# Optimization experiments

Hardware: AMD Instinct MI355X
Metric: run time of the kernel (lower is better)

Reference implementation:

```python
import jax, jax.numpy as jnp
import numpy as np

IGNORE_INDEX = -100


def setup_inputs() -> dict:
    key = jax.random.key(0)
    k1, k2, k3 = jax.random.split(key, 3)
    BT, H, V = 4096, 2048, 32000
    hidden_states = jax.random.normal(k1, (BT, H), dtype=jnp.float32) * 0.02
    weight = jax.random.normal(k2, (V, H), dtype=jnp.float32) * 0.02
    targets = jax.random.randint(k3, (BT,), 0, V, dtype=jnp.int64)
    return {"hidden_states": hidden_states, "weight": weight, "targets": targets}


def reference(hidden_states, weight, targets):
    # Fused lm_head projection + cross-entropy with ignore_index masking,
    # 'mean' reduction over valid rows (matches reduction='mean').
    logits = jnp.einsum('bh,vh->bv', hidden_states, weight).astype(jnp.float32)  # (BT, V)
    lse = jax.nn.logsumexp(logits, axis=-1)  # (BT,)
    safe_tgt = jnp.clip(targets, 0, logits.shape[-1] - 1)
    target_logit = jnp.take_along_axis(logits, safe_tgt[:, None], axis=-1)[:, 0]
    valid = targets != IGNORE_INDEX
    loss_rows = jnp.where(valid, lse - target_logit, 0.0)  # (BT,)
    n_valid = jnp.maximum(valid.sum(), 1)
    return loss_rows.sum() / n_valid.astype(jnp.float32)
```

## Files before the change

kernel.cpp:

```cpp
#include <hip/hip_runtime.h>
#include <hip/hip_bf16.h>

#define BT 4096
#define H  2048
#define V  32000
#define BM 128
#define BN 128
#define BK 128
#define KSTEPS (H / BK)
#define NTILES (V / BN)
#define NWIN   ((NTILES + 7) / 8)
#define IGNORE_INDEX (-100)

typedef int   v8i   __attribute__((ext_vector_type(8)));
typedef float f32x4 __attribute__((ext_vector_type(4)));

#define SCALE_ONE 0x7F7F7F7F
#define UNSCALE   (1.0f / 65536.0f)

__device__ inline void load_lds16(const void* g, void* l) {
  __builtin_amdgcn_global_load_lds(
      (const __attribute__((address_space(1))) unsigned int*)g,
      (__attribute__((address_space(3))) unsigned int*)l,
      16, 0, 0);
}

__global__ __launch_bounds__(256)
void cvt_fp8_kernel(const float* __restrict__ in, unsigned int* __restrict__ out, long n8) {
  long i = (long)blockIdx.x * blockDim.x + threadIdx.x;
  long stride = (long)gridDim.x * blockDim.x;
  for (; i < n8; i += stride) {
    float4 x = ((const float4*)in)[2 * i];
    float4 y = ((const float4*)in)[2 * i + 1];
    int lo = 0, hi = 0;
    lo = __builtin_amdgcn_cvt_pk_fp8_f32(x.x * 256.f, x.y * 256.f, lo, false);
    lo = __builtin_amdgcn_cvt_pk_fp8_f32(x.z * 256.f, x.w * 256.f, lo, true);
    hi = __builtin_amdgcn_cvt_pk_fp8_f32(y.x * 256.f, y.y * 256.f, hi, false);
    hi = __builtin_amdgcn_cvt_pk_fp8_f32(y.z * 256.f, y.w * 256.f, hi, true);
    uint2 p; p.x = (unsigned)lo; p.y = (unsigned)hi;
    ((uint2*)out)[i] = p;
  }
}

__global__ __launch_bounds__(256, 2)
void gemm_lse_kernel(const unsigned char* __restrict__ Af8,
                     const unsigned char* __restrict__ Bf8,
                     const int* __restrict__ tgt,
                     float* __restrict__ pm, float* __restrict__ pl,
                     float* __restrict__ tl) {
  const int bid = blockIdx.x;
  const int wid = bid >> 8;
  const int j   = bid & 255;
  const int nt  = wid * 8 + (j & 7);
  const int mt  = j >> 3;
  if (nt >= NTILES) return;

  __shared__ __align__(16) unsigned char As[BM * BK];
  __shared__ __align__(16) unsigned char Bs[BN * BK];
  __shared__ float red_m[2][BM];
  __shared__ float red_l[2][BM];
  __shared__ int   stgt[BM];

  const int tid  = threadIdx.x;
  const int lane = tid & 63;
  const int w    = tid >> 6;
  const int wr   = w >> 1;
  const int wc   = w & 1;

  const int n0 = nt * BN;
  const int m0 = mt * BM;

  if (tid < BM) stgt[tid] = tgt[m0 + tid];

  const int srow8 = lane >> 3;
  const int kq16  = (((lane & 7) ^ srow8) & 7) * 16;

  const unsigned char* ag = Af8 + (long)(m0 + w * 32 + srow8) * H + kq16;
  const unsigned char* bg = Bf8 + (long)(n0 + w * 32 + srow8) * H + kq16;
  unsigned char* al = (unsigned char*)As + (w * 32) * BK;
  unsigned char* bl = (unsigned char*)Bs + (w * 32) * BK;

  f32x4 acc[4][4];
#pragma unroll
  for (int i = 0; i < 4; ++i)
#pragma unroll
    for (int jj = 0; jj < 4; ++jj)
      acc[i][jj] = (f32x4){0.f, 0.f, 0.f, 0.f};

  const int lm = lane & 15;
  const int q  = lane >> 4;

  for (int ks = 0; ks < KSTEPS; ++ks) {
    const int kk = ks * BK;
#pragma unroll
    for (int s = 0; s < 4; ++s) {
      load_lds16(ag + (long)s * 8 * H + kk, al + s * 8 * BK);
      load_lds16(bg + (long)s * 8 * H + kk, bl + s * 8 * BK);
    }
    __syncthreads();

    union frag { v8i v; int4 h[2]; } af[4], bfr[4];
#pragma unroll
    for (int i = 0; i < 4; ++i) {
      const int row = wr * 64 + i * 16 + lm;
      const unsigned char* base = (const unsigned char*)As + row * BK;
      const int c0 = (2 * q)     ^ (row & 7);
      const int c1 = (2 * q + 1) ^ (row & 7);
      af[i].h[0] = *(const int4*)(base + c0 * 16);
      af[i].h[1] = *(const int4*)(base + c1 * 16);
    }
#pragma unroll
    for (int jj = 0; jj < 4; ++jj) {
      const int row = wc * 64 + jj * 16 + lm;
      const unsigned char* base = (const unsigned char*)Bs + row * BK;
      const int c0 = (2 * q)     ^ (row & 7);
      const int c1 = (2 * q + 1) ^ (row & 7);
      bfr[jj].h[0] = *(const int4*)(base + c0 * 16);
      bfr[jj].h[1] = *(const int4*)(base + c1 * 16);
    }
#pragma unroll
    for (int i = 0; i < 4; ++i)
#pragma unroll
      for (int jj = 0; jj < 4; ++jj)
        acc[i][jj] = __builtin_amdgcn_mfma_scale_f32_16x16x128_f8f6f4(
            af[i].v, bfr[jj].v, acc[i][jj],
            0, 0,
            0, SCALE_ONE,
            0, SCALE_ONE);
    __syncthreads();
  }

#pragma unroll
  for (int i = 0; i < 4; ++i) {
#pragma unroll
    for (int r = 0; r < 4; ++r) {
      int row_local = wr * 64 + i * 16 + q * 4 + r;
      int c = stgt[row_local] - n0 - wc * 64;
      if ((unsigned)c < 64u && (c & 15) == lm) {
        int jj = c >> 4;
        float v = jj == 0 ? acc[i][0][r]
                : jj == 1 ? acc[i][1][r]
                : jj == 2 ? acc[i][2][r]
                :           acc[i][3][r];
        tl[m0 + row_local] = v * UNSCALE;
      }
    }
  }

#pragma unroll
  for (int i = 0; i < 4; ++i) {
#pragma unroll
    for (int r = 0; r < 4; ++r) {
      float v0 = acc[i][0][r] * UNSCALE;
      float v1 = acc[i][1][r] * UNSCALE;
      float v2 = acc[i][2][r] * UNSCALE;
      float v3 = acc[i][3][r] * UNSCALE;
      float mx = fmaxf(fmaxf(v0, v1), fmaxf(v2, v3));
#pragma unroll
      for (int off = 1; off < 16; off <<= 1) mx = fmaxf(mx, __shfl_xor(mx, off));
      float s = __expf(v0 - mx) + __expf(v1 - mx) + __expf(v2 - mx) + __expf(v3 - mx);
#pragma unroll
      for (int off = 1; off < 16; off <<= 1) s += __shfl_xor(s, off);
      if (lm == 0) {
        int row_local = wr * 64 + i * 16 + q * 4 + r;
        red_m[wc][row_local] = mx;
        red_l[wc][row_local] = s;
      }
    }
  }
  __syncthreads();
  if (tid < BM) {
    float ma = red_m[0][tid], mb = red_m[1][tid];
    float M = fmaxf(ma, mb);
    float L = red_l[0][tid] * __expf(ma - M) + red_l[1][tid] * __expf(mb - M);
    long idx = (long)nt * BT + (m0 + tid);
    pm[idx] = M;
    pl[idx] = L;
  }
}

__global__ __launch_bounds__(256)
void row_lse_kernel(const float* __restrict__ pm, const float* __restrict__ pl,
                    const float* __restrict__ tl, const int* __restrict__ tgt,
                    float* __restrict__ rl) {
  int row  = blockIdx.x * 4 + (threadIdx.x >> 6);
  int lane = threadIdx.x & 63;
  float M = -__builtin_inff();
  float L = 0.f;
  for (int t = lane; t < NTILES; t += 64) {
    float m2 = pm[(long)t * BT + row];
    float l2 = pl[(long)t * BT + row];
    float Mn = fmaxf(M, m2);
    L = L * __expf(M - Mn) + l2 * __expf(m2 - Mn);
    M = Mn;
  }
#pragma unroll
  for (int off = 1; off < 64; off <<= 1) {
    float m2 = __shfl_xor(M, off);
    float l2 = __shfl_xor(L, off);
    float Mn = fmaxf(M, m2);
    L = L * __expf(M - Mn) + l2 * __expf(m2 - Mn);
    M = Mn;
  }
  if (lane == 0) {
    float lse = M + logf(L);
    int t = tgt[row];
    rl[row] = (t != IGNORE_INDEX) ? (lse - tl[row]) : 0.f;
  }
}

__global__ __launch_bounds__(256)
void final_kernel(const float* __restrict__ rl, const int* __restrict__ tgt,
                  float* __restrict__ out) {
  __shared__ float ss[4];
  __shared__ float sc[4];
  float s = 0.f, c = 0.f;
  for (int r = threadIdx.x; r < BT; r += 256) {
    s += rl[r];
    c += (tgt[r] != IGNORE_INDEX) ? 1.f : 0.f;
  }
#pragma unroll
  for (int off = 32; off > 0; off >>= 1) {
    s += __shfl_xor(s, off);
    c += __shfl_xor(c, off);
  }
  int w = threadIdx.x >> 6;
  if ((threadIdx.x & 63) == 0) { ss[w] = s; sc[w] = c; }
  __syncthreads();
  if (threadIdx.x == 0) {
    float S = ss[0] + ss[1] + ss[2] + ss[3];
    float C = sc[0] + sc[1] + sc[2] + sc[3];
    out[0] = S / fmaxf(C, 1.f);
  }
}

extern "C" void kernel_launch(void* const* d_in, const int* in_sizes, int n_in,
                              void* d_out, int out_size, void* d_ws, size_t ws_size,
                              hipStream_t stream) {
  const float* hs  = (const float*)d_in[0];
  const float* wt  = (const float*)d_in[1];
  const int*   tgt = (const int*)d_in[2];
  float*       out = (float*)d_out;

  char* ws = (char*)d_ws;
  size_t off = 0;
  auto alloc = [&](size_t bytes) -> void* {
    void* p = ws + off;
    off += (bytes + 255) & ~(size_t)255;
    return p;
  };
  unsigned char* wf8 = (unsigned char*)alloc((size_t)V * H);
  unsigned char* hf8 = (unsigned char*)alloc((size_t)BT * H);
  float* pm = (float*)alloc((size_t)NTILES * BT * 4);
  float* pl = (float*)alloc((size_t)NTILES * BT * 4);
  float* tl = (float*)alloc((size_t)BT * 4);
  float* rl = (float*)alloc((size_t)BT * 4);
  (void)ws_size; (void)in_sizes; (void)n_in; (void)out_size;

  cvt_fp8_kernel<<<8192, 256, 0, stream>>>(wt, (unsigned int*)wf8, (long)V * H / 8);
  cvt_fp8_kernel<<<1024, 256, 0, stream>>>(hs, (unsigned int*)hf8, (long)BT * H / 8);

  gemm_lse_kernel<<<NWIN * 256, 256, 0, stream>>>(hf8, wf8, tgt, pm, pl, tl);

  row_lse_kernel<<<BT / 4, 256, 0, stream>>>(pm, pl, tl, tgt, rl);
  final_kernel<<<1, 256, 0, stream>>>(rl, tgt, out);
}
```

Before: 814.4 us.

## Use 256x256 FP8 GEMM tiles with double-buffered LDS pipelining

The fused GEMM+LSE kernel moves to 256x256 output tiles with 8 waves per block. LDS is double-buffered, and global-to-LDS loads for upcoming K-steps are interleaved with MFMA phases through explicit waitcnt and barrier control plus s_setprio. The grid mapping is also rewritten to spread tiles across XCDs. The aim is to hide load latency and raise data reuse per byte fetched. In exchange, the large LDS footprint limits occupancy to one block per CU, and the hand-written waitcnt counts are fragile.

```diff
diff --git a/kernel.cpp b/kernel.cpp
--- a/kernel.cpp
+++ b/kernel.cpp
@@ -1,15 +1,15 @@
 #include <hip/hip_runtime.h>
-#include <hip/hip_bf16.h>
 
 #define BT 4096
 #define H  2048
 #define V  32000
-#define BM 128
-#define BN 128
-#define BK 128
-#define KSTEPS (H / BK)
+#define BM 256
+#define BN 256
+#define BKB 128
+#define KT (H / BKB)
 #define NTILES (V / BN)
-#define NWIN   ((NTILES + 7) / 8)
+#define MTILES (BT / BM)
+#define NWG (MTILES * NTILES)
 #define IGNORE_INDEX (-100)
 
 typedef int   v8i   __attribute__((ext_vector_type(8)));
@@ -17,6 +17,11 @@
 
 #define SCALE_ONE 0x7F7F7F7F
 #define UNSCALE   (1.0f / 65536.0f)
+
+#define BAR()   __builtin_amdgcn_s_barrier()
+#define LGKM0() asm volatile("s_waitcnt lgkmcnt(0)" ::: "memory")
+#define LGKM8() asm volatile("s_waitcnt lgkmcnt(8)" ::: "memory")
+#define VMC(N)  asm volatile("s_waitcnt vmcnt(" #N ")" ::: "memory")
 
 __device__ inline void load_lds16(const void* g, void* l) {
   __builtin_amdgcn_global_load_lds(
@@ -42,119 +47,213 @@
   }
 }
 
-__global__ __launch_bounds__(256, 2)
+union frag_u { v8i v; int4 h[2]; };
+
+#define MF(C, A, B)                                                         \
+  (C) = __builtin_amdgcn_mfma_scale_f32_16x16x128_f8f6f4(                   \
+      (A).v, (B).v, (C), 0, 0, 0, SCALE_ONE, 0, SCALE_ONE)
+
+__global__ __launch_bounds__(512, 2)
 void gemm_lse_kernel(const unsigned char* __restrict__ Af8,
                      const unsigned char* __restrict__ Bf8,
                      const int* __restrict__ tgt,
                      float* __restrict__ pm, float* __restrict__ pl,
                      float* __restrict__ tl) {
-  const int bid = blockIdx.x;
-  const int wid = bid >> 8;
-  const int j   = bid & 255;
-  const int nt  = wid * 8 + (j & 7);
-  const int mt  = j >> 3;
-  if (nt >= NTILES) return;
-
-  __shared__ __align__(16) unsigned char As[BM * BK];
-  __shared__ __align__(16) unsigned char Bs[BN * BK];
-  __shared__ float red_m[2][BM];
-  __shared__ float red_l[2][BM];
+  __shared__ __align__(16) unsigned char As[2][BM][BKB];
+  __shared__ __align__(16) unsigned char Bs[2][BN][BKB];
+  __shared__ float red_m[4][BM];
+  __shared__ float red_l[4][BM];
   __shared__ int   stgt[BM];
+
+  const int wgid = ((int)blockIdx.x & 7) * (NWG / 8) + ((int)blockIdx.x >> 3);
+  const int mt = wgid & (MTILES - 1);
+  const int nt = wgid / MTILES;
+  const int m0 = mt * BM;
+  const int n0 = nt * BN;
 
   const int tid  = threadIdx.x;
   const int lane = tid & 63;
   const int w    = tid >> 6;
-  const int wr   = w >> 1;
-  const int wc   = w & 1;
-
-  const int n0 = nt * BN;
-  const int m0 = mt * BM;
+  const int wr   = w >> 2;
+  const int wc   = w & 3;
+  const int lm   = lane & 15;
+  const int q    = lane >> 4;
 
   if (tid < BM) stgt[tid] = tgt[m0 + tid];
-
-  const int srow8 = lane >> 3;
-  const int kq16  = (((lane & 7) ^ srow8) & 7) * 16;
-
-  const unsigned char* ag = Af8 + (long)(m0 + w * 32 + srow8) * H + kq16;
-  const unsigned char* bg = Bf8 + (long)(n0 + w * 32 + srow8) * H + kq16;
-  unsigned char* al = (unsigned char*)As + (w * 32) * BK;
-  unsigned char* bl = (unsigned char*)Bs + (w * 32) * BK;
-
-  f32x4 acc[4][4];
-#pragma unroll
-  for (int i = 0; i < 4; ++i)
-#pragma unroll
-    for (int jj = 0; jj < 4; ++jj)
-      acc[i][jj] = (f32x4){0.f, 0.f, 0.f, 0.f};
-
-  const int lm = lane & 15;
-  const int q  = lane >> 4;
-
-  for (int ks = 0; ks < KSTEPS; ++ks) {
-    const int kk = ks * BK;
-#pragma unroll
-    for (int s = 0; s < 4; ++s) {
-      load_lds16(ag + (long)s * 8 * H + kk, al + s * 8 * BK);
-      load_lds16(bg + (long)s * 8 * H + kk, bl + s * 8 * BK);
-    }
-    __syncthreads();
-
-    union frag { v8i v; int4 h[2]; } af[4], bfr[4];
-#pragma unroll
-    for (int i = 0; i < 4; ++i) {
-      const int row = wr * 64 + i * 16 + lm;
-      const unsigned char* base = (const unsigned char*)As + row * BK;
-      const int c0 = (2 * q)     ^ (row & 7);
-      const int c1 = (2 * q + 1) ^ (row & 7);
-      af[i].h[0] = *(const int4*)(base + c0 * 16);
-      af[i].h[1] = *(const int4*)(base + c1 * 16);
-    }
-#pragma unroll
-    for (int jj = 0; jj < 4; ++jj) {
-      const int row = wc * 64 + jj * 16 + lm;
-      const unsigned char* base = (const unsigned char*)Bs + row * BK;
-      const int c0 = (2 * q)     ^ (row & 7);
-      const int c1 = (2 * q + 1) ^ (row & 7);
-      bfr[jj].h[0] = *(const int4*)(base + c0 * 16);
-      bfr[jj].h[1] = *(const int4*)(base + c1 * 16);
-    }
-#pragma unroll
-    for (int i = 0; i < 4; ++i)
-#pragma unroll
-      for (int jj = 0; jj < 4; ++jj)
-        acc[i][jj] = __builtin_amdgcn_mfma_scale_f32_16x16x128_f8f6f4(
-            af[i].v, bfr[jj].v, acc[i][jj],
-            0, 0,
-            0, SCALE_ONE,
-            0, SCALE_ONE);
-    __syncthreads();
-  }
-
-#pragma unroll
-  for (int i = 0; i < 4; ++i) {
+  __syncthreads();
+
+  const int srow = lane >> 3;
+  const int gch  = ((lane & 7) ^ srow) * 16;
+  const unsigned char* aSrc = Af8 + (size_t)(m0 + w * 16 + srow) * H + gch;
+  const unsigned char* bSrc = Bf8 + (size_t)(n0 + w * 16 + srow) * H + gch;
+
+  auto stageA = [&](int buf, int hf, int kt) {
+    const unsigned char* s = aSrc + (size_t)hf * 128 * H + (size_t)kt * BKB;
+    unsigned char* d = &As[buf][hf * 128 + w * 16][0];
+    load_lds16(s, d);
+    load_lds16(s + (size_t)8 * H, d + 8 * BKB);
+  };
+  auto stageB = [&](int buf, int hf, int kt) {
+    const unsigned char* s = bSrc + (size_t)hf * 128 * H + (size_t)kt * BKB;
+    unsigned char* d = &Bs[buf][hf * 128 + w * 16][0];
+    load_lds16(s, d);
+    load_lds16(s + (size_t)8 * H, d + 8 * BKB);
+  };
+
+  const int c0 = ((2 * q)     ^ (lm & 7)) * 16;
+  const int c1 = ((2 * q + 1) ^ (lm & 7)) * 16;
+  const unsigned char* aRdB = &As[0][wr * 128 + lm][0];
+  const unsigned char* bRdB = &Bs[0][wc * 64 + lm][0];
+
+  auto ldA = [&](frag_u& f, int buf, int ai) {
+    const unsigned char* p = aRdB + buf * (BM * BKB) + ai * (16 * BKB);
+    f.h[0] = *(const int4*)(p + c0);
+    f.h[1] = *(const int4*)(p + c1);
+  };
+  auto ldB = [&](frag_u& f, int buf, int bj) {
+    const unsigned char* p = bRdB + buf * (BN * BKB) + bj * (16 * BKB);
+    f.h[0] = *(const int4*)(p + c0);
+    f.h[1] = *(const int4*)(p + c1);
+  };
+
+  f32x4 acc[8][4];
+#pragma unroll
+  for (int a = 0; a < 8; ++a)
+#pragma unroll
+    for (int b = 0; b < 4; ++b) acc[a][b] = (f32x4){0.f, 0.f, 0.f, 0.f};
+
+  frag_u fa0, fa1, fa2, fa3, fb0, fb1, fb2, fb3;
+
+  stageA(0, 0, 0); stageA(0, 1, 0); stageB(0, 0, 0); stageB(0, 1, 0);
+  VMC(4);
+  stageA(1, 0, 1); stageA(1, 1, 1); stageB(1, 0, 1);
+  VMC(6);
+  BAR();
+
+  for (int i = 0; i < 8; ++i) {
+    const int t0 = 2 * i, t1 = 2 * i + 1;
+    const bool pre = (i < 7);
+
+    ldA(fa0, 0, 0); ldA(fa1, 0, 1); ldA(fa2, 0, 2); ldA(fa3, 0, 3);
+    ldB(fb0, 0, 0); ldB(fb1, 0, 1);
+    stageB(1, 1, t1);
+    LGKM8();
+    BAR(); LGKM0();
+    __builtin_amdgcn_s_setprio(1);
+    MF(acc[0][0], fa0, fb0); MF(acc[1][0], fa1, fb0);
+    MF(acc[2][0], fa2, fb0); MF(acc[3][0], fa3, fb0);
+    MF(acc[0][1], fa0, fb1); MF(acc[1][1], fa1, fb1);
+    MF(acc[2][1], fa2, fb1); MF(acc[3][1], fa3, fb1);
+    __builtin_amdgcn_s_setprio(0);
+    BAR();
+
+    ldB(fb2, 0, 2); ldB(fb3, 0, 3);
+    if (pre) stageA(0, 0, t0 + 2);
+    BAR(); LGKM0();
+    __builtin_amdgcn_s_setprio(1);
+    MF(acc[0][2], fa0, fb2); MF(acc[1][2], fa1, fb2);
+    MF(acc[2][2], fa2, fb2); MF(acc[3][2], fa3, fb2);
+    MF(acc[0][3], fa0, fb3); MF(acc[1][3], fa1, fb3);
+    MF(acc[2][3], fa2, fb3); MF(acc[3][3], fa3, fb3);
+    __builtin_amdgcn_s_setprio(0);
+    BAR();
+
+    ldA(fa0, 0, 4); ldA(fa1, 0, 5); ldA(fa2, 0, 6); ldA(fa3, 0, 7);
+    if (pre) stageA(0, 1, t0 + 2);
+    BAR(); LGKM0();
+    __builtin_amdgcn_s_setprio(1);
+    MF(acc[4][0], fa0, fb0); MF(acc[5][0], fa1, fb0);
+    MF(acc[6][0], fa2, fb0); MF(acc[7][0], fa3, fb0);
+    MF(acc[4][1], fa0, fb1); MF(acc[5][1], fa1, fb1);
+    MF(acc[6][1], fa2, fb1); MF(acc[7][1], fa3, fb1);
+    __builtin_amdgcn_s_setprio(0);
+    BAR();
+
+    if (pre) stageB(0, 0, t0 + 2);
+    BAR(); LGKM0();
+    __builtin_amdgcn_s_setprio(1);
+    MF(acc[4][2], fa0, fb2); MF(acc[5][2], fa1, fb2);
+    MF(acc[6][2], fa2, fb2); MF(acc[7][2], fa3, fb2);
+    MF(acc[4][3], fa0, fb3); MF(acc[5][3], fa1, fb3);
+    MF(acc[6][3], fa2, fb3); MF(acc[7][3], fa3, fb3);
+    __builtin_amdgcn_s_setprio(0);
+    if (pre) { VMC(6); } else { VMC(0); }
+    BAR();
+
+    ldA(fa0, 1, 0); ldA(fa1, 1, 1); ldA(fa2, 1, 2); ldA(fa3, 1, 3);
+    ldB(fb0, 1, 0); ldB(fb1, 1, 1);
+    if (pre) stageB(0, 1, t0 + 2);
+    LGKM8();
+    BAR(); LGKM0();
+    __builtin_amdgcn_s_setprio(1);
+    MF(acc[0][0], fa0, fb0); MF(acc[1][0], fa1, fb0);
+    MF(acc[2][0], fa2, fb0); MF(acc[3][0], fa3, fb0);
+    MF(acc[0][1], fa0, fb1); MF(acc[1][1], fa1, fb1);
+    MF(acc[2][1], fa2, fb1); MF(acc[3][1], fa3, fb1);
+    __builtin_amdgcn_s_setprio(0);
+    BAR();
+
+    ldB(fb2, 1, 2); ldB(fb3, 1, 3);
+    if (pre) stageA(1, 0, t1 + 2);
+    BAR(); LGKM0();
+    __builtin_amdgcn_s_setprio(1);
+    MF(acc[0][2], fa0, fb2); MF(acc[1][2], fa1, fb2);
+    MF(acc[2][2], fa2, fb2); MF(acc[3][2], fa3, fb2);
+    MF(acc[0][3], fa0, fb3); MF(acc[1][3], fa1, fb3);
+    MF(acc[2][3], fa2, fb3); MF(acc[3][3], fa3, fb3);
+    __builtin_amdgcn_s_setprio(0);
+    BAR();
+
+    ldA(fa0, 1, 4); ldA(fa1, 1, 5); ldA(fa2, 1, 6); ldA(fa3, 1, 7);
+    if (pre) stageA(1, 1, t1 + 2);
+    BAR(); LGKM0();
+    __builtin_amdgcn_s_setprio(1);
+    MF(acc[4][0], fa0, fb0); MF(acc[5][0], fa1, fb0);
+    MF(acc[6][0], fa2, fb0); MF(acc[7][0], fa3, fb0);
+    MF(acc[4][1], fa0, fb1); MF(acc[5][1], fa1, fb1);
+    MF(acc[6][1], fa2, fb1); MF(acc[7][1], fa3, fb1);
+    __builtin_amdgcn_s_setprio(0);
+    BAR();
+
+    if (pre) stageB(1, 0, t1 + 2);
+    BAR(); LGKM0();
+    __builtin_amdgcn_s_setprio(1);
+    MF(acc[4][2], fa0, fb2); MF(acc[5][2], fa1, fb2);
+    MF(acc[6][2], fa2, fb2); MF(acc[7][2], fa3, fb2);
+    MF(acc[4][3], fa0, fb3); MF(acc[5][3], fa1, fb3);
+    MF(acc[6][3], fa2, fb3); MF(acc[7][3], fa3, fb3);
+    __builtin_amdgcn_s_setprio(0);
+    if (pre) VMC(6);
+    BAR();
+  }
+
+  __syncthreads();
+
+#pragma unroll
+  for (int ai = 0; ai < 8; ++ai) {
 #pragma unroll
     for (int r = 0; r < 4; ++r) {
-      int row_local = wr * 64 + i * 16 + q * 4 + r;
+      int row_local = wr * 128 + ai * 16 + q * 4 + r;
       int c = stgt[row_local] - n0 - wc * 64;
       if ((unsigned)c < 64u && (c & 15) == lm) {
-        int jj = c >> 4;
-        float v = jj == 0 ? acc[i][0][r]
-                : jj == 1 ? acc[i][1][r]
-                : jj == 2 ? acc[i][2][r]
-                :           acc[i][3][r];
+        int bj = c >> 4;
+        float v = bj == 0 ? acc[ai][0][r]
+                : bj == 1 ? acc[ai][1][r]
+                : bj == 2 ? acc[ai][2][r]
+                :           acc[ai][3][r];
         tl[m0 + row_local] = v * UNSCALE;
       }
     }
   }
 
 #pragma unroll
-  for (int i = 0; i < 4; ++i) {
+  for (int ai = 0; ai < 8; ++ai) {
 #pragma unroll
     for (int r = 0; r < 4; ++r) {
-      float v0 = acc[i][0][r] * UNSCALE;
-      float v1 = acc[i][1][r] * UNSCALE;
-      float v2 = acc[i][2][r] * UNSCALE;
-      float v3 = acc[i][3][r] * UNSCALE;
+      float v0 = acc[ai][0][r] * UNSCALE;
+      float v1 = acc[ai][1][r] * UNSCALE;
+      float v2 = acc[ai][2][r] * UNSCALE;
+      float v3 = acc[ai][3][r] * UNSCALE;
       float mx = fmaxf(fmaxf(v0, v1), fmaxf(v2, v3));
 #pragma unroll
       for (int off = 1; off < 16; off <<= 1) mx = fmaxf(mx, __shfl_xor(mx, off));
@@ -162,7 +261,7 @@
 #pragma unroll
       for (int off = 1; off < 16; off <<= 1) s += __shfl_xor(s, off);
       if (lm == 0) {
-        int row_local = wr * 64 + i * 16 + q * 4 + r;
+        int row_local = wr * 128 + ai * 16 + q * 4 + r;
         red_m[wc][row_local] = mx;
         red_l[wc][row_local] = s;
       }
@@ -170,9 +269,12 @@
   }
   __syncthreads();
   if (tid < BM) {
-    float ma = red_m[0][tid], mb = red_m[1][tid];
-    float M = fmaxf(ma, mb);
-    float L = red_l[0][tid] * __expf(ma - M) + red_l[1][tid] * __expf(mb - M);
+    float M = fmaxf(fmaxf(red_m[0][tid], red_m[1][tid]),
+                    fmaxf(red_m[2][tid], red_m[3][tid]));
+    float L = red_l[0][tid] * __expf(red_m[0][tid] - M)
+            + red_l[1][tid] * __expf(red_m[1][tid] - M)
+            + red_l[2][tid] * __expf(red_m[2][tid] - M)
+            + red_l[3][tid] * __expf(red_m[3][tid] - M);
     long idx = (long)nt * BT + (m0 + tid);
     pm[idx] = M;
     pl[idx] = L;
@@ -260,7 +362,7 @@
   cvt_fp8_kernel<<<8192, 256, 0, stream>>>(wt, (unsigned int*)wf8, (long)V * H / 8);
   cvt_fp8_kernel<<<1024, 256, 0, stream>>>(hs, (unsigned int*)hf8, (long)BT * H / 8);
 
-  gemm_lse_kernel<<<NWIN * 256, 256, 0, stream>>>(hf8, wf8, tgt, pm, pl, tl);
+  gemm_lse_kernel<<<NWG, 512, 0, stream>>>(hf8, wf8, tgt, pm, pl, tl);
 
   row_lse_kernel<<<BT / 4, 256, 0, stream>>>(pm, pl, tl, tgt, rl);
   final_kernel<<<1, 256, 0, stream>>>(rl, tgt, out);
```

Result: faster. 763.7 us (-6.2%).
